# Kernel optimization log

Hardware: AMD Instinct MI355X
Metric: run time of the kernel (lower is better)

## Reference

```python
import jax, jax.numpy as jnp
import numpy as np

K = 3  # kernel_size

def _hamming2d(k):
    h = np.hamming(k)
    return (np.outer(h, h)).astype(np.float32)

def setup_inputs() -> dict:
    key = jax.random.key(0)
    k1, k2 = jax.random.split(key)
    x = jax.random.normal(k1, (8, 64, 128, 128), dtype=jnp.float32)
    W = jax.random.normal(k2, (9, 64, 3, 3), dtype=jnp.float32) * 0.001
    b = jnp.zeros((9,), dtype=jnp.float32)
    return {"x": x, "W": W, "b": b}

def reference(x, W, b):
    B, C, H, Wd = x.shape
    # filter generator: 3x3 conv, padding=1 -> (B, K*K, H, W)
    mask = jax.lax.conv_general_dilated(
        x, W, window_strides=(1, 1), padding=((1, 1), (1, 1)),
        dimension_numbers=("NCHW", "OIHW", "NCHW")) + b[None, :, None, None]
    # kernel normalizer: softmax over the K*K taps, hamming reweight, renormalize
    mask = jax.nn.softmax(mask, axis=1)
    ham = jnp.asarray(_hamming2d(K).reshape(-1))  # (K*K,)
    mask = mask * ham[None, :, None, None]
    mask = mask / jnp.sum(mask, axis=1, keepdims=True)
    # carafe (up=1): weighted sum of KxK shifted neighborhoods, reflect-padded.
    pad = K // 2
    xp = jnp.pad(x, ((0, 0), (0, 0), (pad, pad), (pad, pad)), mode="reflect")
    lowpass = jnp.zeros_like(x)
    for idx in range(K * K):
        i, j = divmod(idx, K)
        lowpass = lowpass + xp[:, :, i:i + H, j:j + Wd] * mask[:, idx:idx + 1]
    # highpass = x - lowpass; residual output = x + highpass
    return 2.0 * x - lowpass
```

## Files before the change

### kernel.cpp

```cpp
#include <hip/hip_runtime.h>
#include <hip/hip_fp16.h>


typedef __attribute__((ext_vector_type(8))) short short8;
typedef __attribute__((ext_vector_type(4))) float floatx4;
typedef __attribute__((ext_vector_type(4))) unsigned uint4v;

#define IH 128
#define IW 128
#define CCH 64
#define TSX 16
#define TSY 8
#define TPX 18
#define TPY 10
#define CSH 72

__device__ __forceinline__ unsigned cvtpkh(float a, float b) {
    unsigned r;
    asm("v_cvt_pkrtz_f16_f32 %0, %1, %2" : "=v"(r) : "v"(a), "v"(b));
    return r;
}
__device__ __forceinline__ unsigned pkfma_lo(unsigned x2, unsigned m2, unsigned acc) {
    unsigned d;
    asm("v_pk_fma_f16 %0, %1, %2, %3 op_sel:[0,0,0] op_sel_hi:[1,0,1]"
        : "=v"(d) : "v"(x2), "v"(m2), "v"(acc));
    return d;
}
__device__ __forceinline__ unsigned pkfma_hi(unsigned x2, unsigned m2, unsigned acc) {
    unsigned d;
    asm("v_pk_fma_f16 %0, %1, %2, %3 op_sel:[0,1,0] op_sel_hi:[1,1,1]"
        : "=v"(d) : "v"(x2), "v"(m2), "v"(acc));
    return d;
}
__device__ __forceinline__ unsigned pk2xml(unsigned c2, unsigned two2, unsigned l2) {
    unsigned d;
    asm("v_pk_fma_f16 %0, %1, %2, %3 neg_lo:[0,0,1] neg_hi:[0,0,1]"
        : "=v"(d) : "v"(c2), "v"(two2), "v"(l2));
    return d;
}
__device__ __forceinline__ float h2f_lo(unsigned u) {
    return __half2float(__ushort_as_half((unsigned short)(u & 0xFFFFu)));
}
__device__ __forceinline__ float h2f_hi(unsigned u) {
    return __half2float(__ushort_as_half((unsigned short)(u >> 16)));
}
__device__ __forceinline__ unsigned short f2h(float f) {
    return __half_as_ushort(__float2half(f));
}

__global__ void ahpf_prep(const float* __restrict__ Wg,
                          unsigned short* __restrict__ wsp)
{
    const int i = blockIdx.x * 256 + threadIdx.x;
    if (i >= 18 * 64) return;
    const int s = i >> 6, l = i & 63;
    const int fm = l & 15, fq = l >> 4;
    const int tap = s >> 1, cb = (s & 1) * 32 + fq * 8;
    short8 v = (short8)0;
    if (fm < 9) {
#pragma unroll
        for (int jj = 0; jj < 8; ++jj)
            v[jj] = (short)f2h(Wg[fm * 576 + (cb + jj) * 9 + tap]);
    }
    ((short8*)wsp)[i] = v;
}

template <bool USE_WS>
__global__ __launch_bounds__(128, 2) void ahpf_kernel(
    const float* __restrict__ x, const float* __restrict__ Wg,
    const float* __restrict__ bias, float* __restrict__ out,
    const unsigned short* __restrict__ wsp)
{
    __shared__ __align__(16) unsigned short sx[TPY * TPX * CSH];

    const int tid  = threadIdx.x;
    const int lane = tid & 63;
    const int wv   = tid >> 6;

    const unsigned flat = blockIdx.x + 8u * (blockIdx.y + 16u * blockIdx.z);
    const unsigned nid  = (flat & 7u) * 128u + (flat >> 3);
    const int bx = nid & 7, by = (nid >> 3) & 15, bz = nid >> 7;

    const int ty0 = by * TSY;
    const int tx0 = bx * TSX;
    const size_t hw = (size_t)IH * IW;
    const float* xb = x + (size_t)bz * CCH * hw;

    const int fm = lane & 15;
    const int fq = lane >> 4;

    short8 afr[18];
    if (USE_WS) {
        const short8* wf = (const short8*)wsp;
#pragma unroll
        for (int s = 0; s < 18; ++s) afr[s] = wf[s * 64 + lane];
    } else {
#pragma unroll
        for (int s = 0; s < 18; ++s) {
            short8 a = (short8)0;
            if (fm < 9) {
                const int tap = s >> 1, cb = (s & 1) * 32 + fq * 8;
                const float* wp = Wg + fm * 576 + tap;
#pragma unroll
                for (int jj = 0; jj < 8; ++jj)
                    a[jj] = (short)f2h(wp[(cb + jj) * 9]);
            }
            afr[s] = a;
        }
    }
    float bq[4];
#pragma unroll
    for (int r = 0; r < 4; ++r) {
        const int t = fq * 4 + r;
        bq[r] = (t < 9) ? bias[t] : 0.0f;
    }

    {
        int gx0 = tx0 - 4;
        if (gx0 < 0) gx0 = 0;
        if (gx0 > IW - 24) gx0 = IW - 24;
        const bool xlo = (bx == 0), xhi = (bx == 7);
        const int cg8 = tid & 7;
#pragma unroll
        for (int it = 0; it < 4; ++it) {
            const int s = it * 128 + tid;
            if (s >= 480) break;
            const int u = s >> 3;
            const int y = u / 6, xg = u - 6 * y;
            int gy = ty0 + y - 1;
            gy = gy < 0 ? -gy : (gy >= IH ? 2 * IH - 2 - gy : gy);
            const float* src = xb + (size_t)(cg8 * 8) * hw
                             + (size_t)gy * IW + gx0 + 4 * xg;
            float4 v[8];
#pragma unroll
            for (int jj = 0; jj < 8; ++jj)
                v[jj] = *(const float4*)(src + (size_t)jj * hw);
            const int xbase = gx0 + 4 * xg - tx0 + 1;
#pragma unroll
            for (int e = 0; e < 4; ++e) {
                const float fe[8] = {
                    ((const float*)&v[0])[e], ((const float*)&v[1])[e],
                    ((const float*)&v[2])[e], ((const float*)&v[3])[e],
                    ((const float*)&v[4])[e], ((const float*)&v[5])[e],
                    ((const float*)&v[6])[e], ((const float*)&v[7])[e]};
                uint4v pk;
                pk.x = cvtpkh(fe[0], fe[1]); pk.y = cvtpkh(fe[2], fe[3]);
                pk.z = cvtpkh(fe[4], fe[5]); pk.w = cvtpkh(fe[6], fe[7]);
                const int gxe = gx0 + 4 * xg + e;
                const int xx = xbase + e;
                if (xx >= 0 && xx < TPX)
                    *(uint4v*)&sx[(y * TPX + xx) * CSH + cg8 * 8] = pk;
                if (xlo && gxe == 1)
                    *(uint4v*)&sx[(y * TPX + 0) * CSH + cg8 * 8] = pk;
                if (xhi && gxe == 126)
                    *(uint4v*)&sx[(y * TPX + 17) * CSH + cg8 * 8] = pk;
            }
        }
    }
    __syncthreads();

    const bool border = (bx == 0) | (bx == 7) | (by == 0) | (by == 15);
    const int n = fm;

#define CARAFE_TAP(t, qq, HALF)                                              \
    {                                                                        \
        const uint4v A = *(const uint4v*)&bfr[2 * (t)];                      \
        const uint4v Bv = *(const uint4v*)&bfr[2 * (t) + 1];                 \
        _Pragma("unroll")                                                    \
        for (int u = 0; u < 4; ++u) {                                        \
            l[u]     = pkfma_##HALF(A[u],  qq, l[u]);                        \
            l[4 + u] = pkfma_##HALF(Bv[u], qq, l[4 + u]);                    \
        }                                                                    \
    }

    short8 bfr[18];
#pragma unroll
    for (int rr = 0; rr < 4; ++rr) {
        const int R = wv * 4 + rr;
        const int h = ty0 + R, w = tx0 + n;

        if (rr == 0) {
#pragma unroll
            for (int s = 0; s < 18; ++s) {
                const int tap = s >> 1;
                const int dy = tap / 3 - 1, dx = tap % 3 - 1;
                bfr[s] = *(const short8*)&sx[((R + 1 + dy) * TPX + (n + 1 + dx)) * CSH
                                             + (s & 1) * 32 + fq * 8];
            }
        } else {
#pragma unroll
            for (int s = 0; s < 12; ++s) bfr[s] = bfr[s + 6];
#pragma unroll
            for (int s = 12; s < 18; ++s) {
                const int dx = (s >> 1) % 3 - 1;
                bfr[s] = *(const short8*)&sx[((R + 2) * TPX + (n + 1 + dx)) * CSH
                                             + (s & 1) * 32 + fq * 8];
            }
        }

        floatx4 acc = {0.f, 0.f, 0.f, 0.f};
        if (border) {
#pragma unroll
            for (int s = 0; s < 18; ++s) {
                const int tap = s >> 1;
                const int dy = tap / 3 - 1, dx = tap % 3 - 1;
                const int hy = h + dy, wx = w + dx;
                short8 bb = bfr[s];
                if (hy < 0 || hy >= IH || wx < 0 || wx >= IW) bb = (short8)0;
                acc = __builtin_amdgcn_mfma_f32_16x16x32_f16(afr[s], bb, acc, 0, 0, 0);
            }
        } else {
#pragma unroll
            for (int s = 0; s < 18; ++s)
                acc = __builtin_amdgcn_mfma_f32_16x16x32_f16(afr[s], bfr[s], acc, 0, 0, 0);
        }

        auto hamt = [](int t) {
            const float a = (t / 3 == 1) ? 1.f : 0.08f;
            const float b = (t % 3 == 1) ? 1.f : 0.08f;
            return a * b;
        };
        const int nval = (fq < 2) ? 4 : (fq == 2 ? 1 : 0);
        float e0 = 0, e1 = 0, e2 = 0, e3 = 0, ssum = 0;
        if (nval >= 1) { e0 = __expf(acc[0] + bq[0]) * hamt(fq * 4 + 0); ssum += e0; }
        if (nval >= 4) { e1 = __expf(acc[1] + bq[1]) * hamt(fq * 4 + 1); ssum += e1;
                         e2 = __expf(acc[2] + bq[2]) * hamt(fq * 4 + 2); ssum += e2;
                         e3 = __expf(acc[3] + bq[3]) * hamt(fq * 4 + 3); ssum += e3; }
        ssum += __shfl_xor(ssum, 16);
        ssum += __shfl_xor(ssum, 32);
        const float inv = 1.0f / ssum;

        const unsigned p01 = cvtpkh(e0 * inv, e1 * inv);
        const unsigned p23 = cvtpkh(e2 * inv, e3 * inv);
        const unsigned q0 = (unsigned)__shfl((int)p01, n);
        const unsigned q1 = (unsigned)__shfl((int)p23, n);
        const unsigned q2 = (unsigned)__shfl((int)p01, 16 + n);
        const unsigned q3 = (unsigned)__shfl((int)p23, 16 + n);
        const unsigned q4 = (unsigned)__shfl((int)p01, 32 + n);

        unsigned l[8];
#pragma unroll
        for (int i = 0; i < 8; ++i) l[i] = 0u;
        CARAFE_TAP(0, q0, lo);
        CARAFE_TAP(1, q0, hi);
        CARAFE_TAP(2, q1, lo);
        CARAFE_TAP(3, q1, hi);
        CARAFE_TAP(4, q2, lo);
        CARAFE_TAP(5, q2, hi);
        CARAFE_TAP(6, q3, lo);
        CARAFE_TAP(7, q3, hi);
        CARAFE_TAP(8, q4, lo);

        const uint4v c0 = *(const uint4v*)&bfr[8];
        const uint4v c1 = *(const uint4v*)&bfr[9];
        const unsigned TWO2 = 0x40004000u;
        float* ob = out + (size_t)bz * CCH * hw + (size_t)h * IW + w
                  + (size_t)(8 * fq) * hw;
#pragma unroll
        for (int q = 0; q < 4; ++q) {
            const unsigned oe = pk2xml(c0[q], TWO2, l[q]);
            const unsigned oo = pk2xml(c1[q], TWO2, l[4 + q]);
            ob[(size_t)(2 * q) * hw]          = h2f_lo(oe);
            ob[(size_t)(2 * q + 1) * hw]      = h2f_hi(oe);
            ob[(size_t)(32 + 2 * q) * hw]     = h2f_lo(oo);
            ob[(size_t)(32 + 2 * q + 1) * hw] = h2f_hi(oo);
        }
    }
#undef CARAFE_TAP
}

extern "C" void kernel_launch(void* const* d_in, const int* in_sizes, int n_in,
                              void* d_out, int out_size, void* d_ws, size_t ws_size,
                              hipStream_t stream) {
    const float* x    = (const float*)d_in[0];
    const float* Wg   = (const float*)d_in[1];
    const float* bias = (const float*)d_in[2];
    float* out        = (float*)d_out;
    const int B = in_sizes[0] / (CCH * IH * IW);
    dim3 grid(8, 16, B);

    if (ws_size >= 18 * 64 * 16) {
        unsigned short* wsp = (unsigned short*)d_ws;
        ahpf_prep<<<5, 256, 0, stream>>>(Wg, wsp);
        ahpf_kernel<true><<<grid, dim3(128, 1, 1), 0, stream>>>(x, Wg, bias, out, wsp);
    } else {
        ahpf_kernel<false><<<grid, dim3(128, 1, 1), 0, stream>>>(x, Wg, bias, out, nullptr);
    }
}
```

Measured before the change: 97.69 us.

## Drop weight prep kernel, use rotating row buffer, split MFMA accumulators

Removes the separate weight-packing kernel and its launch, so each block converts the conv weights from global memory itself. That gather now sits after the x tile load is issued, so its latency overlaps with those loads. The row-sliding register copies are replaced by a 4-row rotating buffer indexed at compile time, and the next row's LDS reads are issued right after the MFMAs so they overlap with the softmax and carafe math. The MFMA chain is split across two accumulators to shorten the dependency chain. In exchange, every block redoes the strided weight conversion, and the larger register buffer may raise register pressure under the 2-blocks-per-CU launch bound.

```diff
diff --git a/kernel.cpp b/kernel.cpp
--- a/kernel.cpp
+++ b/kernel.cpp
@@ -48,28 +48,9 @@
     return __half_as_ushort(__float2half(f));
 }
 
-__global__ void ahpf_prep(const float* __restrict__ Wg,
-                          unsigned short* __restrict__ wsp)
-{
-    const int i = blockIdx.x * 256 + threadIdx.x;
-    if (i >= 18 * 64) return;
-    const int s = i >> 6, l = i & 63;
-    const int fm = l & 15, fq = l >> 4;
-    const int tap = s >> 1, cb = (s & 1) * 32 + fq * 8;
-    short8 v = (short8)0;
-    if (fm < 9) {
-#pragma unroll
-        for (int jj = 0; jj < 8; ++jj)
-            v[jj] = (short)f2h(Wg[fm * 576 + (cb + jj) * 9 + tap]);
-    }
-    ((short8*)wsp)[i] = v;
-}
-
-template <bool USE_WS>
 __global__ __launch_bounds__(128, 2) void ahpf_kernel(
     const float* __restrict__ x, const float* __restrict__ Wg,
-    const float* __restrict__ bias, float* __restrict__ out,
-    const unsigned short* __restrict__ wsp)
+    const float* __restrict__ bias, float* __restrict__ out)
 {
     __shared__ __align__(16) unsigned short sx[TPY * TPX * CSH];
 
@@ -88,32 +69,6 @@
 
     const int fm = lane & 15;
     const int fq = lane >> 4;
-
-    short8 afr[18];
-    if (USE_WS) {
-        const short8* wf = (const short8*)wsp;
-#pragma unroll
-        for (int s = 0; s < 18; ++s) afr[s] = wf[s * 64 + lane];
-    } else {
-#pragma unroll
-        for (int s = 0; s < 18; ++s) {
-            short8 a = (short8)0;
-            if (fm < 9) {
-                const int tap = s >> 1, cb = (s & 1) * 32 + fq * 8;
-                const float* wp = Wg + fm * 576 + tap;
-#pragma unroll
-                for (int jj = 0; jj < 8; ++jj)
-                    a[jj] = (short)f2h(wp[(cb + jj) * 9]);
-            }
-            afr[s] = a;
-        }
-    }
-    float bq[4];
-#pragma unroll
-    for (int r = 0; r < 4; ++r) {
-        const int t = fq * 4 + r;
-        bq[r] = (t < 9) ? bias[t] : 0.0f;
-    }
 
     {
         int gx0 = tx0 - 4;
@@ -157,15 +112,41 @@
             }
         }
     }
+
+    short8 afr[18];
+#pragma unroll
+    for (int s = 0; s < 18; ++s) {
+        short8 a = (short8)0;
+        if (fm < 9) {
+            const int tap = s >> 1, cb = (s & 1) * 32 + fq * 8;
+            const float* wp = Wg + fm * 576 + tap;
+#pragma unroll
+            for (int jj = 0; jj < 8; ++jj)
+                a[jj] = (short)f2h(wp[(cb + jj) * 9]);
+        }
+        afr[s] = a;
+    }
+    float bq[4];
+#pragma unroll
+    for (int r = 0; r < 4; ++r) {
+        const int t = fq * 4 + r;
+        bq[r] = (t < 9) ? bias[t] : 0.0f;
+    }
+
     __syncthreads();
 
     const bool border = (bx == 0) | (bx == 7) | (by == 0) | (by == 15);
     const int n = fm;
 
-#define CARAFE_TAP(t, qq, HALF)                                              \
+    short8 rbuf[24];
+#define FR(dy1, dx1, half) rbuf[(((rr + (dy1)) & 3) * 6) + (dx1) * 2 + (half)]
+#define LDSRD(row, dx1, half) \
+    (*(const short8*)&sx[((row) * TPX + (n + (dx1))) * CSH + (half) * 32 + fq * 8])
+
+#define CARAFE_TAP(dy1, dx1, qq, HALF)                                       \
     {                                                                        \
-        const uint4v A = *(const uint4v*)&bfr[2 * (t)];                      \
-        const uint4v Bv = *(const uint4v*)&bfr[2 * (t) + 1];                 \
+        const uint4v A  = *(const uint4v*)&FR(dy1, dx1, 0);                  \
+        const uint4v Bv = *(const uint4v*)&FR(dy1, dx1, 1);                  \
         _Pragma("unroll")                                                    \
         for (int u = 0; u < 4; ++u) {                                        \
             l[u]     = pkfma_##HALF(A[u],  qq, l[u]);                        \
@@ -173,7 +154,6 @@
         }                                                                    \
     }
 
-    short8 bfr[18];
 #pragma unroll
     for (int rr = 0; rr < 4; ++rr) {
         const int R = wv * 4 + rr;
@@ -181,38 +161,48 @@
 
         if (rr == 0) {
 #pragma unroll
-            for (int s = 0; s < 18; ++s) {
-                const int tap = s >> 1;
-                const int dy = tap / 3 - 1, dx = tap % 3 - 1;
-                bfr[s] = *(const short8*)&sx[((R + 1 + dy) * TPX + (n + 1 + dx)) * CSH
-                                             + (s & 1) * 32 + fq * 8];
+            for (int dy1 = 0; dy1 < 3; ++dy1)
+#pragma unroll
+                for (int dx1 = 0; dx1 < 3; ++dx1) {
+                    FR(dy1, dx1, 0) = LDSRD(R + dy1, dx1, 0);
+                    FR(dy1, dx1, 1) = LDSRD(R + dy1, dx1, 1);
+                }
+        }
+
+        floatx4 ac0 = {0.f, 0.f, 0.f, 0.f};
+        floatx4 ac1 = {0.f, 0.f, 0.f, 0.f};
+        if (border) {
+#pragma unroll
+            for (int dy1 = 0; dy1 < 3; ++dy1)
+#pragma unroll
+                for (int dx1 = 0; dx1 < 3; ++dx1) {
+                    const int hy = h + dy1 - 1, wx = w + dx1 - 1;
+                    const bool oob = (hy < 0) | (hy >= IH) | (wx < 0) | (wx >= IW);
+                    short8 b0 = FR(dy1, dx1, 0);
+                    short8 b1 = FR(dy1, dx1, 1);
+                    if (oob) { b0 = (short8)0; b1 = (short8)0; }
+                    const int s2 = 2 * (3 * dy1 + dx1);
+                    ac0 = __builtin_amdgcn_mfma_f32_16x16x32_f16(afr[s2],     b0, ac0, 0, 0, 0);
+                    ac1 = __builtin_amdgcn_mfma_f32_16x16x32_f16(afr[s2 + 1], b1, ac1, 0, 0, 0);
+                }
+        } else {
+#pragma unroll
+            for (int dy1 = 0; dy1 < 3; ++dy1)
+#pragma unroll
+                for (int dx1 = 0; dx1 < 3; ++dx1) {
+                    const int s2 = 2 * (3 * dy1 + dx1);
+                    ac0 = __builtin_amdgcn_mfma_f32_16x16x32_f16(afr[s2],     FR(dy1, dx1, 0), ac0, 0, 0, 0);
+                    ac1 = __builtin_amdgcn_mfma_f32_16x16x32_f16(afr[s2 + 1], FR(dy1, dx1, 1), ac1, 0, 0, 0);
+                }
+        }
+        const floatx4 acc = ac0 + ac1;
+
+        if (rr < 3) {
+#pragma unroll
+            for (int dx1 = 0; dx1 < 3; ++dx1) {
+                rbuf[(((rr + 3) & 3) * 6) + dx1 * 2 + 0] = LDSRD(R + 3, dx1, 0);
+                rbuf[(((rr + 3) & 3) * 6) + dx1 * 2 + 1] = LDSRD(R + 3, dx1, 1);
             }
-        } else {
-#pragma unroll
-            for (int s = 0; s < 12; ++s) bfr[s] = bfr[s + 6];
-#pragma unroll
-            for (int s = 12; s < 18; ++s) {
-                const int dx = (s >> 1) % 3 - 1;
-                bfr[s] = *(const short8*)&sx[((R + 2) * TPX + (n + 1 + dx)) * CSH
-                                             + (s & 1) * 32 + fq * 8];
-            }
-        }
-
-        floatx4 acc = {0.f, 0.f, 0.f, 0.f};
-        if (border) {
-#pragma unroll
-            for (int s = 0; s < 18; ++s) {
-                const int tap = s >> 1;
-                const int dy = tap / 3 - 1, dx = tap % 3 - 1;
-                const int hy = h + dy, wx = w + dx;
-                short8 bb = bfr[s];
-                if (hy < 0 || hy >= IH || wx < 0 || wx >= IW) bb = (short8)0;
-                acc = __builtin_amdgcn_mfma_f32_16x16x32_f16(afr[s], bb, acc, 0, 0, 0);
-            }
-        } else {
-#pragma unroll
-            for (int s = 0; s < 18; ++s)
-                acc = __builtin_amdgcn_mfma_f32_16x16x32_f16(afr[s], bfr[s], acc, 0, 0, 0);
         }
 
         auto hamt = [](int t) {
@@ -241,18 +231,18 @@
         unsigned l[8];
 #pragma unroll
         for (int i = 0; i < 8; ++i) l[i] = 0u;
-        CARAFE_TAP(0, q0, lo);
-        CARAFE_TAP(1, q0, hi);
-        CARAFE_TAP(2, q1, lo);
-        CARAFE_TAP(3, q1, hi);
-        CARAFE_TAP(4, q2, lo);
-        CARAFE_TAP(5, q2, hi);
-        CARAFE_TAP(6, q3, lo);
-        CARAFE_TAP(7, q3, hi);
-        CARAFE_TAP(8, q4, lo);
-
-        const uint4v c0 = *(const uint4v*)&bfr[8];
-        const uint4v c1 = *(const uint4v*)&bfr[9];
+        CARAFE_TAP(0, 0, q0, lo);
+        CARAFE_TAP(0, 1, q0, hi);
+        CARAFE_TAP(0, 2, q1, lo);
+        CARAFE_TAP(1, 0, q1, hi);
+        CARAFE_TAP(1, 1, q2, lo);
+        CARAFE_TAP(1, 2, q2, hi);
+        CARAFE_TAP(2, 0, q3, lo);
+        CARAFE_TAP(2, 1, q3, hi);
+        CARAFE_TAP(2, 2, q4, lo);
+
+        const uint4v c0 = *(const uint4v*)&FR(1, 1, 0);
+        const uint4v c1 = *(const uint4v*)&FR(1, 1, 1);
         const unsigned TWO2 = 0x40004000u;
         float* ob = out + (size_t)bz * CCH * hw + (size_t)h * IW + w
                   + (size_t)(8 * fq) * hw;
@@ -267,6 +257,8 @@
         }
     }
 #undef CARAFE_TAP
+#undef LDSRD
+#undef FR
 }
 
 extern "C" void kernel_launch(void* const* d_in, const int* in_sizes, int n_in,
@@ -278,12 +270,5 @@
     float* out        = (float*)d_out;
     const int B = in_sizes[0] / (CCH * IH * IW);
     dim3 grid(8, 16, B);
-
-    if (ws_size >= 18 * 64 * 16) {
-        unsigned short* wsp = (unsigned short*)d_ws;
-        ahpf_prep<<<5, 256, 0, stream>>>(Wg, wsp);
-        ahpf_kernel<true><<<grid, dim3(128, 1, 1), 0, stream>>>(x, Wg, bias, out, wsp);
-    } else {
-        ahpf_kernel<false><<<grid, dim3(128, 1, 1), 0, stream>>>(x, Wg, bias, out, nullptr);
-    }
-}
+    ahpf_kernel<<<grid, dim3(128, 1, 1), 0, stream>>>(x, Wg, bias, out);
+}
```

Result: slower. 111.9 us (+14.5%).
